# Performance work log

Measured on AMD Instinct MI355X. Metric: run time of the kernel, lower is better.

## Reference

```python
import jax, jax.numpy as jnp
import numpy as np

NUM_EMBEDDINGS = 1024
EMBEDDING_DIM = 256
COMMITMENT_COST = 0.25


def setup_inputs() -> dict:
    key = jax.random.key(0)
    k1, k2 = jax.random.split(key)
    inputs = jax.random.normal(k1, (64, 32, 32, EMBEDDING_DIM), dtype=jnp.float32)
    embed = jax.random.normal(k2, (NUM_EMBEDDINGS, EMBEDDING_DIM), dtype=jnp.float32)
    return {"inputs": inputs, "embed": embed}


def reference(inputs, embed):
    # Eval-mode forward (no EMA buffer mutation), use_ema=True loss branch.
    input_shape = inputs.shape
    flat = inputs.reshape(-1, EMBEDDING_DIM)  # [N, d]
    distances = (
        jnp.sum(flat * flat, axis=1, keepdims=True)
        + jnp.sum(embed * embed, axis=1)
        - 2.0 * jnp.matmul(flat, embed.T)
    )
    encoding_indices = jnp.argmin(distances, axis=1)  # [N]
    # Gather codebook rows (equivalent to one-hot @ embed)
    quantized = embed[encoding_indices].reshape(input_shape)
    # use_ema branch: loss = commitment * mse(stop_grad(quantized), inputs)
    e_latent_loss = jnp.mean((jax.lax.stop_gradient(quantized) - inputs) ** 2)
    loss = COMMITMENT_COST * e_latent_loss
    # Straight-through estimator
    quantized_st = inputs + jax.lax.stop_gradient(quantized - inputs)
    # Perplexity from code usage histogram (== mean of one-hot encodings)
    n_tokens = flat.shape[0]
    counts = jax.ops.segment_sum(
        jnp.ones((n_tokens,), dtype=jnp.float32), encoding_indices,
        num_segments=NUM_EMBEDDINGS)
    avg_probs = counts / n_tokens
    perplexity = jnp.exp(-jnp.sum(avg_probs * jnp.log(avg_probs + 1e-10)))
    return quantized_st, loss, perplexity, encoding_indices
```

## Files before the change

kernel.cpp:

```cpp
#include <hip/hip_runtime.h>

#define NTOK 65536
#define DIM 256
#define KC 1024
#define EPS 0.08f

typedef __attribute__((ext_vector_type(8))) _Float16 f16x8;
typedef __attribute__((ext_vector_type(8))) unsigned short u16x8;
typedef __attribute__((ext_vector_type(4))) float f32x4;

static __device__ __forceinline__ unsigned short f16bits(float f) {
  _Float16 h = (_Float16)f;
  return __builtin_bit_cast(unsigned short, h);
}

__global__ __launch_bounds__(256) void vq_prep_e(const float* __restrict__ e,
                                                 unsigned short* __restrict__ eg,
                                                 float* __restrict__ esq,
                                                 int* __restrict__ hist,
                                                 int* __restrict__ fixCount) {
  const int gid = blockIdx.x * 256 + threadIdx.x;
  const int t = gid >> 5;
  const int o = gid & 31;
  const float4 v0 = *reinterpret_cast<const float4*>(&e[t * DIM + o * 8]);
  const float4 v1 = *reinterpret_cast<const float4*>(&e[t * DIM + o * 8 + 4]);
  u16x8 u;
  u[0] = f16bits(v0.x); u[1] = f16bits(v0.y); u[2] = f16bits(v0.z); u[3] = f16bits(v0.w);
  u[4] = f16bits(v1.x); u[5] = f16bits(v1.y); u[6] = f16bits(v1.z); u[7] = f16bits(v1.w);
  const int ctk = t >> 6, njj = (t >> 4) & 3, col = t & 15;
  const int s = o >> 2, kq = o & 3;
  char* dst = (char*)eg + ((ctk * 32 + s * 4 + njj) << 10) + ((kq * 16 + col) << 4);
  *reinterpret_cast<u16x8*>(dst) = u;
  float p = v0.x * v0.x + v0.y * v0.y + v0.z * v0.z + v0.w * v0.w +
            v1.x * v1.x + v1.y * v1.y + v1.z * v1.z + v1.w * v1.w;
#pragma unroll
  for (int m = 16; m > 0; m >>= 1) p += __shfl_xor(p, m, 64);
  if (o == 0) esq[t] = p;
  if (blockIdx.x < 4) hist[blockIdx.x * 256 + threadIdx.x] = 0;
  if (gid == 0) *fixCount = 0;
}

__global__ __launch_bounds__(256) void vq_prep_x(const float* __restrict__ x,
                                                 unsigned short* __restrict__ xg,
                                                 float* __restrict__ xsq) {
  const int gid = blockIdx.x * 256 + threadIdx.x;
  const int t = gid >> 5;
  const int o = gid & 31;
  const float4 v0 = *reinterpret_cast<const float4*>(&x[t * DIM + o * 8]);
  const float4 v1 = *reinterpret_cast<const float4*>(&x[t * DIM + o * 8 + 4]);
  u16x8 u;
  u[0] = f16bits(v0.x); u[1] = f16bits(v0.y); u[2] = f16bits(v0.z); u[3] = f16bits(v0.w);
  u[4] = f16bits(v1.x); u[5] = f16bits(v1.y); u[6] = f16bits(v1.z); u[7] = f16bits(v1.w);
  const int s = o >> 2, kq = o & 3;
  char* dst = (char*)xg + (((t >> 4) * 8 + s) << 10) + ((kq * 16 + (t & 15)) << 4);
  *reinterpret_cast<u16x8*>(dst) = u;
  float p = v0.x * v0.x + v0.y * v0.y + v0.z * v0.z + v0.w * v0.w +
            v1.x * v1.x + v1.y * v1.y + v1.z * v1.z + v1.w * v1.w;
#pragma unroll
  for (int m = 16; m > 0; m >>= 1) p += __shfl_xor(p, m, 64);
  if (o == 0) xsq[t] = p;
}

__global__ __launch_bounds__(256, 3) void vq_argmin(
    const unsigned short* __restrict__ xg, const unsigned short* __restrict__ eg,
    const float* __restrict__ esq, float* __restrict__ rV1,
    unsigned int* __restrict__ rI1, float* __restrict__ rV2,
    unsigned int* __restrict__ rI2) {
  const int lane = threadIdx.x & 63, w = threadIdx.x >> 6;
  const int col = lane & 15, kq = lane >> 4;
  const int cp = blockIdx.x & 7, tb = blockIdx.x >> 3;
  const int cbase = cp * 128 + w * 32;
  const int ctk = cbase >> 6;
  const int njb = (w & 1) * 2;
  const int pw = cp * 4 + w;

  f16x8 ae[8][2];
#pragma unroll
  for (int s = 0; s < 8; ++s)
#pragma unroll
    for (int cg = 0; cg < 2; ++cg)
      ae[s][cg] = *reinterpret_cast<const f16x8*>(
          (const char*)eg + ((ctk * 32 + s * 4 + njb + cg) << 10) + (lane << 4));
  float esr[2][4];
#pragma unroll
  for (int cg = 0; cg < 2; ++cg)
#pragma unroll
    for (int r = 0; r < 4; ++r)
      esr[cg][r] = esq[cbase + cg * 16 + kq * 4 + r];

  for (int i = 0; i < 16; ++i) {
    const int tsub = tb * 16 + i;
    f32x4 acc[2];
    acc[0] = (f32x4){0.f, 0.f, 0.f, 0.f};
    acc[1] = (f32x4){0.f, 0.f, 0.f, 0.f};
#pragma unroll
    for (int s = 0; s < 8; ++s) {
      const f16x8 bx = *reinterpret_cast<const f16x8*>(
          (const char*)xg + ((tsub * 8 + s) << 10) + (lane << 4));
      acc[0] = __builtin_amdgcn_mfma_f32_16x16x32_f16(ae[s][0], bx, acc[0], 0, 0, 0);
      acc[1] = __builtin_amdgcn_mfma_f32_16x16x32_f16(ae[s][1], bx, acc[1], 0, 0, 0);
    }
    float v1 = 3.4e38f, v2 = 3.4e38f, v3 = 3.4e38f;
    int i1 = 0, i2 = 0;
#pragma unroll
    for (int cg = 0; cg < 2; ++cg)
#pragma unroll
      for (int r = 0; r < 4; ++r) {
        const int code = cbase + cg * 16 + kq * 4 + r;
        const float d = fmaf(-2.f, acc[cg][r], esr[cg][r]);
        if (d < v1) { v3 = v2; v2 = v1; i2 = i1; v1 = d; i1 = code; }
        else if (d < v2) { v3 = v2; v2 = d; i2 = code; }
        else if (d < v3) { v3 = d; }
      }
#pragma unroll
    for (int m = 16; m <= 32; m <<= 1) {
      const float ov1 = __shfl_xor(v1, m, 64);
      const float ov2 = __shfl_xor(v2, m, 64);
      const float ov3 = __shfl_xor(v3, m, 64);
      const int oi1 = __shfl_xor(i1, m, 64);
      const int oi2 = __shfl_xor(i2, m, 64);
      const bool oW = (ov1 < v1) || (ov1 == v1 && oi1 < i1);
      const float wv1 = oW ? ov1 : v1, wv2 = oW ? ov2 : v2, wv3 = oW ? ov3 : v3;
      const int wi1 = oW ? oi1 : i1, wi2 = oW ? oi2 : i2;
      const float lv1 = oW ? v1 : ov1, lv2 = oW ? v2 : ov2;
      const int li1 = oW ? i1 : oi1;
      const bool w2 = (wv2 < lv1) || (wv2 == lv1 && wi2 < li1);
      v1 = wv1; i1 = wi1;
      v2 = w2 ? wv2 : lv1;
      i2 = w2 ? wi2 : li1;
      v3 = w2 ? fminf(wv3, lv1) : fminf(wv2, lv2);
    }
    if (kq == 0) {
      const int rb = pw * NTOK + tsub * 16 + col;
      rV1[rb] = v1;
      rI1[rb] = (unsigned)i1 | ((v3 - v1 < EPS) ? 0x80000000u : 0u);
      rV2[rb] = v2;
      rI2[rb] = (unsigned)i2;
    }
  }
}

__global__ __launch_bounds__(256) void vq_finish1(
    const float* __restrict__ rV1, const unsigned int* __restrict__ rI1,
    const float* __restrict__ rV2, const unsigned int* __restrict__ rI2,
    const float* __restrict__ xsq, float* __restrict__ outIdxF,
    float* __restrict__ bestDist, int* __restrict__ hist,
    int* __restrict__ fixCount, unsigned int* __restrict__ fixList) {
  const int t = blockIdx.x * 256 + threadIdx.x;
  float m1 = 3.4e38f, m2 = 3.4e38f, m3 = 3.4e38f;
  int mi1 = 0x7FFFFFFF, mi2 = 0x7FFFFFFF;
  float minFlagV1 = 3.4e38f;
#pragma unroll
  for (int p = 0; p < 32; ++p) {
    const int rb = p * NTOK + t;
    const float a1 = rV1[rb];
    const unsigned u1 = rI1[rb];
    const float a2 = rV2[rb];
    const int ai2 = (int)rI2[rb];
    const int ai1 = (int)(u1 & 0x7FFFFFFFu);
    if (u1 >> 31) minFlagV1 = fminf(minFlagV1, a1);
    if (a1 < m1 || (a1 == m1 && ai1 < mi1)) {
      m3 = m2; m2 = m1; mi2 = mi1; m1 = a1; mi1 = ai1;
    } else if (a1 < m2 || (a1 == m2 && ai1 < mi2)) {
      m3 = m2; m2 = a1; mi2 = ai1;
    } else if (a1 < m3) m3 = a1;
    if (a2 < m1 || (a2 == m1 && ai2 < mi1)) {
      m3 = m2; m2 = m1; mi2 = mi1; m1 = a2; mi1 = ai2;
    } else if (a2 < m2 || (a2 == m2 && ai2 < mi2)) {
      m3 = m2; m2 = a2; mi2 = ai2;
    } else if (a2 < m3) m3 = a2;
  }
  outIdxF[t] = (float)mi1;
  bestDist[t] = xsq[t] + m1;
  atomicAdd(&hist[mi1], 1);
  if (m2 - m1 < EPS) {
    const bool full = (m3 - m1 < EPS) || (minFlagV1 - m1 < EPS);
    const int p = atomicAdd(fixCount, 1);
    fixList[p * 2] = (unsigned)t | (full ? 0x80000000u : 0u);
    fixList[p * 2 + 1] = (unsigned)(mi2 & 0x3FF);
  }
}

__global__ __launch_bounds__(256) void vq_gather(
    const float* __restrict__ e, const float* __restrict__ outIdxF,
    float* __restrict__ outQ) {
  const int lane = threadIdx.x & 63, w = threadIdx.x >> 6;
  const int t0 = blockIdx.x * 64 + w * 16;
#pragma unroll
  for (int i = 0; i < 16; ++i) {
    const int t = t0 + i;
    const int id = (int)outIdxF[t];
    const float4 q = reinterpret_cast<const float4*>(&e[id * DIM])[lane];
    reinterpret_cast<float4*>(&outQ[t * DIM])[lane] = q;
  }
}

__global__ __launch_bounds__(256) void vq_fixup(
    const float* __restrict__ x, const float* __restrict__ e,
    const int* __restrict__ fixCount, const unsigned int* __restrict__ fixList,
    float* __restrict__ outIdxF, float* __restrict__ outQ,
    float* __restrict__ bestDist, int* __restrict__ hist) {
  const int n = *fixCount;
  const int tid = threadIdx.x;
  __shared__ float xrow[256];
  __shared__ float rv[4];
  __shared__ int ri[4];
  __shared__ int sOld, sFi;
  for (int it = blockIdx.x; it < n; it += gridDim.x) {
    const unsigned e0 = fixList[it * 2];
    const int t = (int)(e0 & 0x3FFFFFFFu);
    const bool full = (e0 >> 31) != 0u;
    if (!full) {
      if (tid < 64) {
        const int i1 = (int)outIdxF[t];
        const int i2 = (int)fixList[it * 2 + 1];
        const float4 xv = reinterpret_cast<const float4*>(&x[t * DIM])[tid];
        const float4 e1 = reinterpret_cast<const float4*>(&e[i1 * DIM])[tid];
        const float4 e2 = reinterpret_cast<const float4*>(&e[i2 * DIM])[tid];
        float d1 = (xv.x - e1.x) * (xv.x - e1.x) + (xv.y - e1.y) * (xv.y - e1.y) +
                   (xv.z - e1.z) * (xv.z - e1.z) + (xv.w - e1.w) * (xv.w - e1.w);
        float d2 = (xv.x - e2.x) * (xv.x - e2.x) + (xv.y - e2.y) * (xv.y - e2.y) +
                   (xv.z - e2.z) * (xv.z - e2.z) + (xv.w - e2.w) * (xv.w - e2.w);
#pragma unroll
        for (int m = 32; m > 0; m >>= 1) {
          d1 += __shfl_xor(d1, m, 64);
          d2 += __shfl_xor(d2, m, 64);
        }
        const bool swap2 = (d2 < d1) || (d2 == d1 && i2 < i1);
        const int wIdx = swap2 ? i2 : i1;
        const float wD = swap2 ? d2 : d1;
        if (tid == 0) {
          bestDist[t] = wD;
          if (wIdx != i1) {
            atomicSub(&hist[i1], 1);
            atomicAdd(&hist[wIdx], 1);
            outIdxF[t] = (float)wIdx;
          }
        }
        if (swap2) {
          const float4 q = reinterpret_cast<const float4*>(&e[wIdx * DIM])[tid];
          reinterpret_cast<float4*>(&outQ[t * DIM])[tid] = q;
        }
      }
    } else {
      __syncthreads();
      if (tid < 64) ((float4*)xrow)[tid] = ((const float4*)&x[t * DIM])[tid];
      __syncthreads();
      float bv = 3.4e38f; int bi = 0;
      for (int c = tid; c < KC; c += 256) {
        float s = 0.f;
#pragma unroll
        for (int d = 0; d < DIM; d += 4) {
          const float4 ev = *(const float4*)&e[c * DIM + d];
          const float d0 = xrow[d] - ev.x, d1 = xrow[d + 1] - ev.y;
          const float d2 = xrow[d + 2] - ev.z, d3 = xrow[d + 3] - ev.w;
          s += d0 * d0 + d1 * d1 + d2 * d2 + d3 * d3;
        }
        if (s < bv) { bv = s; bi = c; }
      }
#pragma unroll
      for (int m = 1; m <= 32; m <<= 1) {
        const float ob = __shfl_xor(bv, m, 64);
        const int oi = __shfl_xor(bi, m, 64);
        if (ob < bv || (ob == bv && oi < bi)) { bv = ob; bi = oi; }
      }
      const int lane = tid & 63, wv = tid >> 6;
      if (lane == 0) { rv[wv] = bv; ri[wv] = bi; }
      __syncthreads();
      if (tid == 0) {
        float fb = rv[0]; int fi = ri[0];
        for (int k = 1; k < 4; ++k)
          if (rv[k] < fb || (rv[k] == fb && ri[k] < fi)) { fb = rv[k]; fi = ri[k]; }
        sOld = (int)outIdxF[t];
        sFi = fi;
        bestDist[t] = fb;
        if (fi != sOld) {
          atomicSub(&hist[sOld], 1);
          atomicAdd(&hist[fi], 1);
          outIdxF[t] = (float)fi;
        }
      }
      __syncthreads();
      if (sFi != sOld) outQ[t * DIM + tid] = e[sFi * DIM + tid];
      __syncthreads();
    }
  }
}

__global__ __launch_bounds__(1024) void vq_final(
    const int* __restrict__ hist, const float* __restrict__ bestDist,
    float* __restrict__ outLoss, float* __restrict__ outPerp) {
  const int tid = threadIdx.x;
  float ls = 0.f;
  for (int i = 0; i < 64; ++i) ls += bestDist[tid + i * 1024];
  const float p = (float)hist[tid] * (1.f / 65536.f);
  float ent = p * logf(p + 1e-10f);
#pragma unroll
  for (int o = 32; o > 0; o >>= 1) {
    ls += __shfl_down(ls, o, 64);
    ent += __shfl_down(ent, o, 64);
  }
  __shared__ float lbuf[16], ebuf[16];
  const int lane = tid & 63, wv = tid >> 6;
  if (lane == 0) { lbuf[wv] = ls; ebuf[wv] = ent; }
  __syncthreads();
  if (tid == 0) {
    float L = 0.f, E = 0.f;
    for (int i = 0; i < 16; ++i) { L += lbuf[i]; E += ebuf[i]; }
    *outLoss = 0.25f * (L / 16777216.f);
    *outPerp = expf(-E);
  }
}

extern "C" void kernel_launch(void* const* d_in, const int* in_sizes, int n_in,
                              void* d_out, int out_size, void* d_ws, size_t ws_size,
                              hipStream_t stream) {
  const float* x = (const float*)d_in[0];
  const float* e = (const float*)d_in[1];
  float* out = (float*)d_out;
  float* outQ = out;
  float* outLoss = out + 16777216;
  float* outPerp = out + 16777217;
  float* outIdxF = out + 16777218;

  unsigned short* xg = (unsigned short*)d_out;
  float* rV1 = out + 8388608;
  unsigned int* rI1 = (unsigned int*)(out + 10485760);
  float* rV2 = out + 12582912;
  unsigned int* rI2 = (unsigned int*)(out + 14680064);

  char* ws = (char*)d_ws;
  int*   hist     = (int*)ws;
  float* esq      = (float*)(ws + 4096);
  float* xsq      = (float*)(ws + 8192);
  float* bestDist = (float*)(ws + 270336);
  int*   fixCount = (int*)(ws + 532480);
  unsigned int* fixList = (unsigned int*)(ws + 532496);
  unsigned short* e_f16 = (unsigned short*)(ws + 1056784);

  vq_prep_e<<<128, 256, 0, stream>>>(e, e_f16, esq, hist, fixCount);
  vq_prep_x<<<8192, 256, 0, stream>>>(x, xg, xsq);
  vq_argmin<<<2048, 256, 0, stream>>>(xg, e_f16, esq, rV1, rI1, rV2, rI2);
  vq_finish1<<<256, 256, 0, stream>>>(rV1, rI1, rV2, rI2, xsq, outIdxF,
                                      bestDist, hist, fixCount, fixList);
  vq_gather<<<1024, 256, 0, stream>>>(e, outIdxF, outQ);
  vq_fixup<<<256, 256, 0, stream>>>(x, e, fixCount, fixList, outIdxF, outQ,
                                    bestDist, hist);
  vq_final<<<1, 1024, 0, stream>>>(hist, bestDist, outLoss, outPerp);
}
```

Baseline: 200.5 us.

## Pack distance and code index into sortable keys for top-3 argmin reduction

Replaces separate value/index pairs with a single 32-bit sortable key that encodes the distance with its low 10 bits replaced by the code index. The top-3 merge in both the argmin kernel and the finish kernel then uses integer min/max with no branches, and intermediate storage drops from four arrays to three. It also raises occupancy (launch bounds 3 to 4), remaps blocks so that adjacent blocks share x tiles, and loads the codebook fragments with inline asm followed by a scheduling barrier. Truncating the low mantissa bits loses distance precision, which the EPS-based fixup pass is relied on to absorb.

New measurement: 178.4 us. 1.12x faster.

```diff
diff --git a/kernel.cpp b/kernel.cpp
--- a/kernel.cpp
+++ b/kernel.cpp
@@ -12,6 +12,16 @@
 static __device__ __forceinline__ unsigned short f16bits(float f) {
   _Float16 h = (_Float16)f;
   return __builtin_bit_cast(unsigned short, h);
+}
+static __device__ __forceinline__ unsigned packKey(float d, int code) {
+  unsigned b = __float_as_uint(d);
+  b = ((int)b < 0) ? ~b : (b | 0x80000000u);
+  return (b & ~1023u) | (unsigned)code;
+}
+static __device__ __forceinline__ float decKey(unsigned k) {
+  unsigned b = k & ~1023u;
+  b = (b & 0x80000000u) ? (b ^ 0x80000000u) : ~b;
+  return __uint_as_float(b);
 }
 
 __global__ __launch_bounds__(256) void vq_prep_e(const float* __restrict__ e,
@@ -61,14 +71,16 @@
   if (o == 0) xsq[t] = p;
 }
 
-__global__ __launch_bounds__(256, 3) void vq_argmin(
+__global__ __launch_bounds__(256, 4) void vq_argmin(
     const unsigned short* __restrict__ xg, const unsigned short* __restrict__ eg,
-    const float* __restrict__ esq, float* __restrict__ rV1,
-    unsigned int* __restrict__ rI1, float* __restrict__ rV2,
-    unsigned int* __restrict__ rI2) {
+    const float* __restrict__ esq, unsigned int* __restrict__ rK1,
+    unsigned int* __restrict__ rK2, unsigned int* __restrict__ rK3) {
   const int lane = threadIdx.x & 63, w = threadIdx.x >> 6;
   const int col = lane & 15, kq = lane >> 4;
-  const int cp = blockIdx.x & 7, tb = blockIdx.x >> 3;
+  const int g = blockIdx.x & 7;
+  const int j = blockIdx.x >> 3;
+  const int cp = j & 7;
+  const int tb = g * 32 + (j >> 3);
   const int cbase = cp * 128 + w * 32;
   const int ctk = cbase >> 6;
   const int njb = (w & 1) * 2;
@@ -78,15 +90,20 @@
 #pragma unroll
   for (int s = 0; s < 8; ++s)
 #pragma unroll
-    for (int cg = 0; cg < 2; ++cg)
-      ae[s][cg] = *reinterpret_cast<const f16x8*>(
-          (const char*)eg + ((ctk * 32 + s * 4 + njb + cg) << 10) + (lane << 4));
+    for (int cg = 0; cg < 2; ++cg) {
+      const char* ap =
+          (const char*)eg + ((ctk * 32 + s * 4 + njb + cg) << 10) + (lane << 4);
+      asm volatile("global_load_dwordx4 %0, %1, off"
+                   : "=v"(ae[s][cg]) : "v"(ap) : "memory");
+    }
   float esr[2][4];
 #pragma unroll
   for (int cg = 0; cg < 2; ++cg)
 #pragma unroll
     for (int r = 0; r < 4; ++r)
       esr[cg][r] = esq[cbase + cg * 16 + kq * 4 + r];
+  asm volatile("s_waitcnt vmcnt(0)" ::: "memory");
+  __builtin_amdgcn_sched_barrier(0);
 
   for (int i = 0; i < 16; ++i) {
     const int tsub = tb * 16 + i;
@@ -100,84 +117,65 @@
       acc[0] = __builtin_amdgcn_mfma_f32_16x16x32_f16(ae[s][0], bx, acc[0], 0, 0, 0);
       acc[1] = __builtin_amdgcn_mfma_f32_16x16x32_f16(ae[s][1], bx, acc[1], 0, 0, 0);
     }
-    float v1 = 3.4e38f, v2 = 3.4e38f, v3 = 3.4e38f;
-    int i1 = 0, i2 = 0;
+    unsigned k1 = 0xFFFFFFFFu, k2 = 0xFFFFFFFFu, k3 = 0xFFFFFFFFu;
 #pragma unroll
     for (int cg = 0; cg < 2; ++cg)
 #pragma unroll
       for (int r = 0; r < 4; ++r) {
         const int code = cbase + cg * 16 + kq * 4 + r;
-        const float d = fmaf(-2.f, acc[cg][r], esr[cg][r]);
-        if (d < v1) { v3 = v2; v2 = v1; i2 = i1; v1 = d; i1 = code; }
-        else if (d < v2) { v3 = v2; v2 = d; i2 = code; }
-        else if (d < v3) { v3 = d; }
+        const unsigned k = packKey(fmaf(-2.f, acc[cg][r], esr[cg][r]), code);
+        if (k < k1) { k3 = k2; k2 = k1; k1 = k; }
+        else if (k < k2) { k3 = k2; k2 = k; }
+        else if (k < k3) { k3 = k; }
       }
 #pragma unroll
     for (int m = 16; m <= 32; m <<= 1) {
-      const float ov1 = __shfl_xor(v1, m, 64);
-      const float ov2 = __shfl_xor(v2, m, 64);
-      const float ov3 = __shfl_xor(v3, m, 64);
-      const int oi1 = __shfl_xor(i1, m, 64);
-      const int oi2 = __shfl_xor(i2, m, 64);
-      const bool oW = (ov1 < v1) || (ov1 == v1 && oi1 < i1);
-      const float wv1 = oW ? ov1 : v1, wv2 = oW ? ov2 : v2, wv3 = oW ? ov3 : v3;
-      const int wi1 = oW ? oi1 : i1, wi2 = oW ? oi2 : i2;
-      const float lv1 = oW ? v1 : ov1, lv2 = oW ? v2 : ov2;
-      const int li1 = oW ? i1 : oi1;
-      const bool w2 = (wv2 < lv1) || (wv2 == lv1 && wi2 < li1);
-      v1 = wv1; i1 = wi1;
-      v2 = w2 ? wv2 : lv1;
-      i2 = w2 ? wi2 : li1;
-      v3 = w2 ? fminf(wv3, lv1) : fminf(wv2, lv2);
+      const unsigned o1 = __shfl_xor((int)k1, m, 64);
+      const unsigned o2 = __shfl_xor((int)k2, m, 64);
+      const unsigned o3 = __shfl_xor((int)k3, m, 64);
+      const unsigned t1 = max(k1, o1), lo2 = min(k2, o2);
+      const unsigned nm1 = min(k1, o1);
+      const unsigned nm2 = min(t1, lo2);
+      const unsigned nm3 = min(min(max(t1, lo2), max(k2, o2)), min(k3, o3));
+      k1 = nm1; k2 = nm2; k3 = nm3;
     }
     if (kq == 0) {
       const int rb = pw * NTOK + tsub * 16 + col;
-      rV1[rb] = v1;
-      rI1[rb] = (unsigned)i1 | ((v3 - v1 < EPS) ? 0x80000000u : 0u);
-      rV2[rb] = v2;
-      rI2[rb] = (unsigned)i2;
+      rK1[rb] = k1; rK2[rb] = k2; rK3[rb] = k3;
     }
   }
 }
 
 __global__ __launch_bounds__(256) void vq_finish1(
-    const float* __restrict__ rV1, const unsigned int* __restrict__ rI1,
-    const float* __restrict__ rV2, const unsigned int* __restrict__ rI2,
-    const float* __restrict__ xsq, float* __restrict__ outIdxF,
-    float* __restrict__ bestDist, int* __restrict__ hist,
-    int* __restrict__ fixCount, unsigned int* __restrict__ fixList) {
+    const unsigned int* __restrict__ rK1, const unsigned int* __restrict__ rK2,
+    const unsigned int* __restrict__ rK3, const float* __restrict__ xsq,
+    float* __restrict__ outIdxF, float* __restrict__ bestDist,
+    int* __restrict__ hist, int* __restrict__ fixCount,
+    unsigned int* __restrict__ fixList) {
   const int t = blockIdx.x * 256 + threadIdx.x;
-  float m1 = 3.4e38f, m2 = 3.4e38f, m3 = 3.4e38f;
-  int mi1 = 0x7FFFFFFF, mi2 = 0x7FFFFFFF;
-  float minFlagV1 = 3.4e38f;
+  unsigned m1 = 0xFFFFFFFFu, m2 = 0xFFFFFFFFu, m3 = 0xFFFFFFFFu;
+  unsigned minFlagK1 = 0xFFFFFFFFu;
 #pragma unroll
   for (int p = 0; p < 32; ++p) {
     const int rb = p * NTOK + t;
-    const float a1 = rV1[rb];
-    const unsigned u1 = rI1[rb];
-    const float a2 = rV2[rb];
-    const int ai2 = (int)rI2[rb];
-    const int ai1 = (int)(u1 & 0x7FFFFFFFu);
-    if (u1 >> 31) minFlagV1 = fminf(minFlagV1, a1);
-    if (a1 < m1 || (a1 == m1 && ai1 < mi1)) {
-      m3 = m2; m2 = m1; mi2 = mi1; m1 = a1; mi1 = ai1;
-    } else if (a1 < m2 || (a1 == m2 && ai1 < mi2)) {
-      m3 = m2; m2 = a1; mi2 = ai1;
-    } else if (a1 < m3) m3 = a1;
-    if (a2 < m1 || (a2 == m1 && ai2 < mi1)) {
-      m3 = m2; m2 = m1; mi2 = mi1; m1 = a2; mi1 = ai2;
-    } else if (a2 < m2 || (a2 == m2 && ai2 < mi2)) {
-      m3 = m2; m2 = a2; mi2 = ai2;
-    } else if (a2 < m3) m3 = a2;
-  }
+    const unsigned a1 = rK1[rb], a2 = rK2[rb], a3 = rK3[rb];
+    if (decKey(a3) - decKey(a1) < EPS) minFlagK1 = min(minFlagK1, a1);
+    const unsigned t1 = max(m1, a1), lo2 = min(m2, a2);
+    const unsigned nm1 = min(m1, a1);
+    const unsigned nm2 = min(t1, lo2);
+    const unsigned nm3 = min(min(max(t1, lo2), max(m2, a2)), min(m3, a3));
+    m1 = nm1; m2 = nm2; m3 = nm3;
+  }
+  const int mi1 = (int)(m1 & 1023u);
+  const float d1 = decKey(m1);
   outIdxF[t] = (float)mi1;
-  bestDist[t] = xsq[t] + m1;
+  bestDist[t] = xsq[t] + d1;
   atomicAdd(&hist[mi1], 1);
-  if (m2 - m1 < EPS) {
-    const bool full = (m3 - m1 < EPS) || (minFlagV1 - m1 < EPS);
+  if (decKey(m2) - d1 < EPS) {
+    const bool full = (decKey(m3) - d1 < EPS) || (decKey(minFlagK1) - d1 < EPS);
     const int p = atomicAdd(fixCount, 1);
     fixList[p * 2] = (unsigned)t | (full ? 0x80000000u : 0u);
-    fixList[p * 2 + 1] = (unsigned)(mi2 & 0x3FF);
+    fixList[p * 2 + 1] = m2 & 1023u;
   }
 }
 
@@ -324,10 +322,9 @@
   float* outIdxF = out + 16777218;
 
   unsigned short* xg = (unsigned short*)d_out;
-  float* rV1 = out + 8388608;
-  unsigned int* rI1 = (unsigned int*)(out + 10485760);
-  float* rV2 = out + 12582912;
-  unsigned int* rI2 = (unsigned int*)(out + 14680064);
+  unsigned int* rK1 = (unsigned int*)(out + 8388608);
+  unsigned int* rK2 = (unsigned int*)(out + 10485760);
+  unsigned int* rK3 = (unsigned int*)(out + 12582912);
 
   char* ws = (char*)d_ws;
   int*   hist     = (int*)ws;
@@ -340,9 +337,9 @@
 
   vq_prep_e<<<128, 256, 0, stream>>>(e, e_f16, esq, hist, fixCount);
   vq_prep_x<<<8192, 256, 0, stream>>>(x, xg, xsq);
-  vq_argmin<<<2048, 256, 0, stream>>>(xg, e_f16, esq, rV1, rI1, rV2, rI2);
-  vq_finish1<<<256, 256, 0, stream>>>(rV1, rI1, rV2, rI2, xsq, outIdxF,
-                                      bestDist, hist, fixCount, fixList);
+  vq_argmin<<<2048, 256, 0, stream>>>(xg, e_f16, esq, rK1, rK2, rK3);
+  vq_finish1<<<256, 256, 0, stream>>>(rK1, rK2, rK3, xsq, outIdxF, bestDist,
+                                      hist, fixCount, fixList);
   vq_gather<<<1024, 256, 0, stream>>>(e, outIdxF, outQ);
   vq_fixup<<<256, 256, 0, stream>>>(x, e, fixCount, fixList, outIdxF, outQ,
                                     bestDist, hist);
```
